# Performance work log

Measured on AMD Instinct MI355X. Metric: run time of the kernel, lower is better.

The kernel has to match this reference:

```python
import jax, jax.numpy as jnp
import numpy as np

D_MODEL = 1024
N_HEADS = 16
HEAD_DIM = D_MODEL // N_HEADS
SCALE = HEAD_DIM ** -0.5
MIN_VAL = jnp.finfo(jnp.float32).min


def setup_inputs() -> dict:
    key = jax.random.key(0)
    ks = jax.random.split(key, 7)
    B, T = 1, 2048
    s = D_MODEL ** -0.5
    return {
        "x": jax.random.normal(ks[0], (B, T, D_MODEL), dtype=jnp.float32),
        "Wq": jax.random.normal(ks[1], (D_MODEL, D_MODEL), dtype=jnp.float32) * s,
        "Wk1": jax.random.normal(ks[2], (D_MODEL, D_MODEL), dtype=jnp.float32) * s,
        "Wk2": jax.random.normal(ks[3], (D_MODEL, D_MODEL), dtype=jnp.float32) * s,
        "Wv": jax.random.normal(ks[4], (D_MODEL, D_MODEL), dtype=jnp.float32) * s,
        "Wo": jax.random.normal(ks[5], (D_MODEL, D_MODEL), dtype=jnp.float32) * s,
        "lambda_logit": jnp.zeros((N_HEADS,), dtype=jnp.float32),  # logit(0.5)=0
    }


def _split_heads(y):
    B, T, _ = y.shape
    return y.reshape(B, T, N_HEADS, HEAD_DIM).transpose(0, 2, 1, 3)  # [B,H,T,hd]


def reference(x, Wq, Wk1, Wk2, Wv, Wo, lambda_logit):
    B, T, _ = x.shape
    q = _split_heads(x @ Wq.T)
    k1 = _split_heads(x @ Wk1.T)
    k2 = _split_heads(x @ Wk2.T)
    v = _split_heads(x @ Wv.T)

    s1 = jnp.einsum("bhqd,bhkd->bhqk", q, k1) * SCALE
    s2 = jnp.einsum("bhqd,bhkd->bhqk", q, k2) * SCALE

    causal = jnp.arange(T)[None, :] <= jnp.arange(T)[:, None]  # [T,T] keep mask
    s1 = jnp.where(causal[None, None], s1, MIN_VAL)
    s2 = jnp.where(causal[None, None], s2, MIN_VAL)

    attn_exp = jax.nn.softmax(s1, axis=-1)
    attn_noise = jax.nn.softmax(s2, axis=-1)
    lam = jax.nn.sigmoid(lambda_logit)[None, :, None, None]
    attn = attn_exp - lam * attn_noise
    denom = jnp.maximum(jnp.sum(jnp.abs(attn), axis=-1, keepdims=True), 1e-6)
    attn = attn / denom

    out = jnp.einsum("bhqk,bhkd->bhqd", attn, v)
    out = out.transpose(0, 2, 1, 3).reshape(B, T, D_MODEL)
    return out @ Wo.T
```

## Files before the change

kernel.cpp:

```cpp
#include <hip/hip_runtime.h>

#define T_SEQ 2048
#define DM 1024
#define NH 16
#define HD 64
#define SC2 0.1803368801111731f
#define LS 72

typedef unsigned short u16;
typedef unsigned int u32;
typedef __attribute__((ext_vector_type(8))) short bf16x8;
typedef __attribute__((ext_vector_type(4))) float f32x4;

static __device__ __forceinline__ f32x4 mfma16(bf16x8 a, bf16x8 b, f32x4 c) {
    return __builtin_amdgcn_mfma_f32_16x16x32_bf16(a, b, c, 0, 0, 0);
}
static __device__ __forceinline__ float bf2f(u16 u) {
    union { u32 i; float f; } v; v.i = ((u32)u) << 16; return v.f;
}
static __device__ __forceinline__ u16 f2bf(float f) {
    union { float f; u32 i; } v; v.f = f;
    u32 x = v.i;
    x += 0x7FFFu + ((x >> 16) & 1u);
    return (u16)(x >> 16);
}
static __device__ __forceinline__ u16 f2bf_t(float f) {
    union { float f; u32 i; } v; v.f = f;
    return (u16)(v.i >> 16);
}
static __device__ __forceinline__ u32 pk2(float lo, float hi) {
    return (u32)f2bf(lo) | ((u32)f2bf(hi) << 16);
}
static __device__ __forceinline__ float qsum16(float v) {
#pragma unroll
    for (int o = 1; o < 16; o <<= 1) v += __shfl_xor(v, o, 64);
    return v;
}
static __device__ __forceinline__ float ex2(float x) {
    return __builtin_amdgcn_exp2f(x);
}

static __device__ __forceinline__ void gl16(const u16* g, u16* l) {
    __builtin_amdgcn_global_load_lds(
        (const __attribute__((address_space(1))) void*)g,
        (__attribute__((address_space(3))) void*)l,
        16, 0, 0);
}

template <int NISS>
static __device__ __forceinline__ void stage_async(const u16* src, size_t row0,
                                                   size_t lds_, size_t col0,
                                                   u16* dst, int tid) {
#pragma unroll
    for (int it = 0; it < NISS; it++) {
        int r = it * 32 + (tid >> 3);
        int cg = (tid & 7) ^ (r & 7);
        gl16(&src[(row0 + r) * lds_ + col0 + cg * 8], &dst[(it * 256 + tid) * 8]);
    }
}
static __device__ __forceinline__ bf16x8 frag(const u16* buf, int R, int co) {
    return *(const bf16x8*)(&buf[R * 64 + co]);
}

__global__ __launch_bounds__(256) void detect_dtype(const u16* __restrict__ x,
                                                    int* __restrict__ flag) {
    __shared__ int tot;
    const int tid = threadIdx.x;
    if (tid == 0) tot = 0;
    __syncthreads();
    int c = 0;
#pragma unroll
    for (int i = 0; i < 4; i++) {
        u16 v = x[2 * (tid * 4 + i)];
        int e = (v >> 7) & 0xFF;
        c += (e >= 110 && e <= 140) ? 1 : 0;
    }
    atomicAdd(&tot, c);
    __syncthreads();
    if (tid == 0) *flag = (tot >= 512) ? 1 : 0;
}

__global__ __launch_bounds__(256) void cvt_bf16(
    const int* __restrict__ flag,
    const float* __restrict__ x, const float* __restrict__ wq,
    const float* __restrict__ wk1, const float* __restrict__ wk2,
    const float* __restrict__ wv, const float* __restrict__ wo,
    u16* __restrict__ xc, u16* __restrict__ wqc, u16* __restrict__ wk1c,
    u16* __restrict__ wk2c, u16* __restrict__ wvc, u16* __restrict__ woc) {
    if (*flag) return;
    const int b = blockIdx.x;
    const int tid = threadIdx.x;
    const float* src;
    u16* dst;
    int rel;
    if (b < 1024)      { src = x;   dst = xc;   rel = b; }
    else if (b < 1536) { src = wq;  dst = wqc;  rel = b - 1024; }
    else if (b < 2048) { src = wk1; dst = wk1c; rel = b - 1536; }
    else if (b < 2560) { src = wk2; dst = wk2c; rel = b - 2048; }
    else if (b < 3072) { src = wv;  dst = wvc;  rel = b - 2560; }
    else               { src = wo;  dst = woc;  rel = b - 3072; }
    size_t idx = (size_t)rel * 2048 + (size_t)tid * 8;
    const float* s = src + idx;
    uint4 a = *(const uint4*)s;
    uint4 bq = *(const uint4*)(s + 4);
    const float* af = (const float*)&a;
    const float* bf = (const float*)&bq;
    uint4 r;
    r.x = pk2(af[0], af[1]); r.y = pk2(af[2], af[3]);
    r.z = pk2(bf[0], bf[1]); r.w = pk2(bf[2], bf[3]);
    *(uint4*)(dst + idx) = r;
}

__global__ __launch_bounds__(256) void qkv_gemm(
    const int* __restrict__ flag,
    const void* __restrict__ x0, const void* __restrict__ wq0,
    const void* __restrict__ wk10, const void* __restrict__ wk20,
    const void* __restrict__ wv0,
    const u16* __restrict__ xc, const u16* __restrict__ wqc,
    const u16* __restrict__ wk1c, const u16* __restrict__ wk2c,
    const u16* __restrict__ wvc,
    u16* __restrict__ qd, u16* __restrict__ k1d, u16* __restrict__ k2d,
    u16* __restrict__ vtd) {
    __shared__ __align__(16) u16 As[2][128 * 64];
    __shared__ __align__(16) u16 Bs[2][128 * 64];

    const int f = *flag;
    const int tid = threadIdx.x;
    const int w = blockIdx.x >> 3;
    const int n0 = (blockIdx.x & 7) * 128;
    const int m0 = blockIdx.y * 128;
    const u16* xb = f ? (const u16*)x0 : xc;
    const u16* Bb;
    if (w == 0)      Bb = f ? (const u16*)wq0  : wqc;
    else if (w == 1) Bb = f ? (const u16*)wk10 : wk1c;
    else if (w == 2) Bb = f ? (const u16*)wk20 : wk2c;
    else             Bb = f ? (const u16*)wv0  : wvc;

    const int lane = tid & 63, wave = tid >> 6;
    const int lr = lane & 15, quad = lane >> 4;
    const int wm = (wave >> 1) * 64, wn = (wave & 1) * 64;
    const int sw = lr & 7;

    f32x4 acc[4][4];
#pragma unroll
    for (int i = 0; i < 4; i++)
#pragma unroll
        for (int j = 0; j < 4; j++) acc[i][j] = (f32x4){0.f, 0.f, 0.f, 0.f};

    stage_async<4>(xb, m0, DM, 0, As[0], tid);
    stage_async<4>(Bb, n0, DM, 0, Bs[0], tid);
    for (int k0 = 0; k0 < DM; k0 += 64) {
        const int cur = (k0 >> 6) & 1;
        __syncthreads();
        if (k0 + 64 < DM) {
            stage_async<4>(xb, m0, DM, k0 + 64, As[cur ^ 1], tid);
            stage_async<4>(Bb, n0, DM, k0 + 64, Bs[cur ^ 1], tid);
        }
#pragma unroll
        for (int kk = 0; kk < 2; kk++) {
            const int co = ((kk * 4 + quad) ^ sw) * 8;
            bf16x8 af[4], bfr[4];
#pragma unroll
            for (int i = 0; i < 4; i++) af[i] = frag(As[cur], wm + i * 16 + lr, co);
#pragma unroll
            for (int j = 0; j < 4; j++) bfr[j] = frag(Bs[cur], wn + j * 16 + lr, co);
#pragma unroll
            for (int i = 0; i < 4; i++)
#pragma unroll
                for (int j = 0; j < 4; j++) acc[i][j] = mfma16(af[i], bfr[j], acc[i][j]);
        }
    }

#pragma unroll
    for (int i = 0; i < 4; i++)
#pragma unroll
        for (int j = 0; j < 4; j++)
#pragma unroll
            for (int r = 0; r < 4; r++) {
                int t = m0 + wm + i * 16 + quad * 4 + r;
                int o = n0 + wn + j * 16 + lr;
                float val = acc[i][j][r];
                if (w == 0) val *= SC2;
                u16 vbits = f2bf(val);
                int hh = o >> 6, d0 = o & 63;
                if (w == 3)
                    vtd[((size_t)hh * HD + d0) * T_SEQ + t] = vbits;
                else
                    ((w == 0) ? qd : (w == 1) ? k1d : k2d)[((size_t)hh * T_SEQ + t) * HD + d0] = vbits;
            }
}

#define ATTN_MAP_COMMON()                                     \
    const int tid = threadIdx.x;                              \
    const int lane = tid & 63, wave = tid >> 6;               \
    const int lr = lane & 15, quad = lane >> 4;               \
    const int wm = wave * 16;                                 \
    const int sw = lr & 7;

__global__ __launch_bounds__(256) void attn_a(
    const u16* __restrict__ qg, const u16* __restrict__ k1g,
    const u16* __restrict__ k2g, float* __restrict__ zp) {
    __shared__ __align__(16) u16 k1s[64 * 64];
    __shared__ __align__(16) u16 k2s[64 * 64];
    const int b = blockIdx.x;
    const int x = b & 7;
    const int g = b >> 3;
    const int hl = g >> 7;
    const int par = (g >> 5) & 3;
    const int bi = g & 31;
    const int qt = (bi < 16) ? bi : 47 - bi;
    const int h = x * 2 + hl;
    const int t0 = qt * 64;
    ATTN_MAP_COMMON();

    const u16* qh = qg + (size_t)h * T_SEQ * HD;
    const u16* k1h = k1g + (size_t)h * T_SEQ * HD;
    const u16* k2h = k2g + (size_t)h * T_SEQ * HD;

    bf16x8 aq[2];
#pragma unroll
    for (int kk = 0; kk < 2; kk++)
        aq[kk] = *(const bf16x8*)(&qh[(size_t)(t0 + wm + lr) * HD + kk * 32 + quad * 8]);

    float z1a[4] = {0.f, 0.f, 0.f, 0.f}, z2a[4] = {0.f, 0.f, 0.f, 0.f};

    for (int kt = par; kt <= qt; kt += 4) {
        __syncthreads();
        stage_async<2>(k1h, (size_t)kt * 64, HD, 0, k1s, tid);
        stage_async<2>(k2h, (size_t)kt * 64, HD, 0, k2s, tid);
        __syncthreads();

        f32x4 sa[4], sb[4];
#pragma unroll
        for (int j = 0; j < 4; j++) { sa[j] = (f32x4){0.f,0.f,0.f,0.f}; sb[j] = (f32x4){0.f,0.f,0.f,0.f}; }
#pragma unroll
        for (int kk = 0; kk < 2; kk++) {
            const int co = ((kk * 4 + quad) ^ sw) * 8;
#pragma unroll
            for (int j = 0; j < 4; j++) {
                sa[j] = mfma16(aq[kk], frag(k1s, j * 16 + lr, co), sa[j]);
                sb[j] = mfma16(aq[kk], frag(k2s, j * 16 + lr, co), sb[j]);
            }
        }

        if (kt < qt) {
#pragma unroll
            for (int r = 0; r < 4; r++)
#pragma unroll
                for (int j = 0; j < 4; j++) {
                    z1a[r] += ex2(sa[j][r]);
                    z2a[r] += ex2(sb[j][r]);
                }
        } else {
#pragma unroll
            for (int r = 0; r < 4; r++) {
                const int grow = t0 + wm + quad * 4 + r;
#pragma unroll
                for (int j = 0; j < 4; j++) {
                    int gcol = kt * 64 + j * 16 + lr;
                    if (gcol <= grow) {
                        z1a[r] += ex2(sa[j][r]);
                        z2a[r] += ex2(sb[j][r]);
                    }
                }
            }
        }
    }

#pragma unroll
    for (int r = 0; r < 4; r++) {
        float s1 = qsum16(z1a[r]);
        float s2 = qsum16(z2a[r]);
        if (lr == 0) {
            int row = t0 + wm + quad * 4 + r;
            zp[((size_t)(par * 2 + 0) * NH + h) * T_SEQ + row] = s1;
            zp[((size_t)(par * 2 + 1) * NH + h) * T_SEQ + row] = s2;
        }
    }
}

__global__ __launch_bounds__(256) void attn_b(
    const u16* __restrict__ qg, const u16* __restrict__ k1g,
    const u16* __restrict__ k2g, const u16* __restrict__ vtg,
    const float* __restrict__ zp, const void* __restrict__ lamsrc,
    const int* __restrict__ flag,
    float* __restrict__ dpart, u16* __restrict__ opart) {
    __shared__ __align__(16) u16 k1s[64 * 64];
    __shared__ __align__(16) u16 k2s[64 * 64];
    __shared__ __align__(16) u16 vs[64 * 64];
    __shared__ __align__(16) u16 ps[4][16 * LS];
    const int b = blockIdx.x;
    const int x = b & 7;
    const int g = b >> 3;
    const int hl = g >> 6;
    const int par = (g >> 5) & 1;
    const int bi = g & 31;
    const int qt = (bi < 16) ? bi : 47 - bi;
    const int h = x * 2 + hl;
    const int t0 = qt * 64;
    ATTN_MAP_COMMON();

    const int f = *flag;
    float lamlogit = f ? bf2f(((const u16*)lamsrc)[h]) : ((const float*)lamsrc)[h];
    const float lam = 1.0f / (1.0f + __expf(-lamlogit));

    const u16* qh = qg + (size_t)h * T_SEQ * HD;
    const u16* k1h = k1g + (size_t)h * T_SEQ * HD;
    const u16* k2h = k2g + (size_t)h * T_SEQ * HD;
    const u16* vh = vtg + (size_t)h * HD * T_SEQ;

    bf16x8 aq[2];
#pragma unroll
    for (int kk = 0; kk < 2; kk++)
        aq[kk] = *(const bf16x8*)(&qh[(size_t)(t0 + wm + lr) * HD + kk * 32 + quad * 8]);

    float z1l[4], z2l[4];
#pragma unroll
    for (int r = 0; r < 4; r++) {
        int row = t0 + wm + quad * 4 + r;
        float z1 = 0.f, z2 = 0.f;
#pragma unroll
        for (int p = 0; p < 4; p++) {
            z1 += zp[((size_t)(p * 2 + 0) * NH + h) * T_SEQ + row];
            z2 += zp[((size_t)(p * 2 + 1) * NH + h) * T_SEQ + row];
        }
        z1l[r] = -__log2f(z1);
        z2l[r] = __log2f(lam) - __log2f(z2);
    }

    f32x4 oac[4];
#pragma unroll
    for (int j = 0; j < 4; j++) oac[j] = (f32x4){0.f, 0.f, 0.f, 0.f};
    float dacc[4] = {0.f, 0.f, 0.f, 0.f};

    for (int kt = par; kt <= qt; kt += 2) {
        __syncthreads();
        stage_async<2>(k1h, (size_t)kt * 64, HD, 0, k1s, tid);
        stage_async<2>(k2h, (size_t)kt * 64, HD, 0, k2s, tid);
        stage_async<2>(vh, 0, T_SEQ, (size_t)kt * 64, vs, tid);
        __syncthreads();

        f32x4 sa[4], sb[4];
#pragma unroll
        for (int j = 0; j < 4; j++) { sa[j] = (f32x4){0.f,0.f,0.f,0.f}; sb[j] = (f32x4){0.f,0.f,0.f,0.f}; }
#pragma unroll
        for (int kk = 0; kk < 2; kk++) {
            const int co = ((kk * 4 + quad) ^ sw) * 8;
#pragma unroll
            for (int j = 0; j < 4; j++) {
                sa[j] = mfma16(aq[kk], frag(k1s, j * 16 + lr, co), sa[j]);
                sb[j] = mfma16(aq[kk], frag(k2s, j * 16 + lr, co), sb[j]);
            }
        }

        if (kt < qt) {
#pragma unroll
            for (int r = 0; r < 4; r++)
#pragma unroll
                for (int j = 0; j < 4; j++) {
                    float p = ex2(sa[j][r] + z1l[r]) - ex2(sb[j][r] + z2l[r]);
                    dacc[r] += fabsf(p);
                    ps[wave][(quad * 4 + r) * LS + j * 16 + lr] = f2bf_t(p);
                }
        } else {
#pragma unroll
            for (int r = 0; r < 4; r++) {
                const int grow = t0 + wm + quad * 4 + r;
#pragma unroll
                for (int j = 0; j < 4; j++) {
                    int gcol = kt * 64 + j * 16 + lr;
                    float p = 0.f;
                    if (gcol <= grow)
                        p = ex2(sa[j][r] + z1l[r]) - ex2(sb[j][r] + z2l[r]);
                    dacc[r] += fabsf(p);
                    ps[wave][(quad * 4 + r) * LS + j * 16 + lr] = f2bf_t(p);
                }
            }
        }

#pragma unroll
        for (int kk = 0; kk < 2; kk++) {
            bf16x8 pa = *(const bf16x8*)(&ps[wave][lr * LS + kk * 32 + quad * 8]);
            const int co = ((kk * 4 + quad) ^ sw) * 8;
#pragma unroll
            for (int j = 0; j < 4; j++)
                oac[j] = mfma16(pa, frag(vs, j * 16 + lr, co), oac[j]);
        }
    }

#pragma unroll
    for (int r = 0; r < 4; r++) {
        float ds = qsum16(dacc[r]);
        if (lr == 0) {
            int row = t0 + wm + quad * 4 + r;
            dpart[((size_t)par * NH + h) * T_SEQ + row] = ds;
        }
    }
#pragma unroll
    for (int j = 0; j < 4; j++)
#pragma unroll
        for (int r = 0; r < 4; r++) {
            int row = t0 + wm + quad * 4 + r;
            opart[(size_t)par * T_SEQ * DM + (size_t)row * DM + h * HD + j * 16 + lr] =
                f2bf(oac[j][r]);
        }
}

__global__ __launch_bounds__(256) void normalize_o(
    const u16* __restrict__ opart, const float* __restrict__ dpart,
    u16* __restrict__ ao) {
    int g = blockIdx.x * 256 + threadIdx.x;
    int t = g >> 7;
    int cc = g & 127;
    int d0 = cc * 8;
    int h = d0 >> 6;
    float dsum = dpart[(size_t)h * T_SEQ + t] + dpart[(size_t)(NH + h) * T_SEQ + t];
    float rs = 1.f / fmaxf(dsum, 1e-6f);
    uint4 a = *(const uint4*)(&opart[(size_t)t * DM + d0]);
    uint4 bqq = *(const uint4*)(&opart[(size_t)T_SEQ * DM + (size_t)t * DM + d0]);
    const u32* au = (const u32*)&a;
    const u32* bu = (const u32*)&bqq;
    uint4 out;
    u32* ou = (u32*)&out;
#pragma unroll
    for (int i = 0; i < 4; i++) {
        float lo = (bf2f((u16)(au[i] & 0xFFFF)) + bf2f((u16)(bu[i] & 0xFFFF))) * rs;
        float hi = (bf2f((u16)(au[i] >> 16)) + bf2f((u16)(bu[i] >> 16))) * rs;
        ou[i] = pk2(lo, hi);
    }
    *(uint4*)(&ao[(size_t)t * DM + d0]) = out;
}

__global__ __launch_bounds__(256) void out_gemm(
    const u16* __restrict__ ab, const void* __restrict__ wo0,
    const u16* __restrict__ woc, const int* __restrict__ flag,
    void* __restrict__ outp) {
    __shared__ __align__(16) u16 As[2][64 * 64];
    __shared__ __align__(16) u16 Bs[2][64 * 64];

    const int f = *flag;
    const u16* wb = f ? (const u16*)wo0 : woc;
    const int n0 = blockIdx.x * 64;
    const int m0 = blockIdx.y * 64;
    const int tid = threadIdx.x;
    const int lane = tid & 63, wave = tid >> 6;
    const int lr = lane & 15, quad = lane >> 4;
    const int wm = (wave >> 1) * 32, wn = (wave & 1) * 32;
    const int sw = lr & 7;

    f32x4 acc[2][2];
#pragma unroll
    for (int i = 0; i < 2; i++)
#pragma unroll
        for (int j = 0; j < 2; j++) acc[i][j] = (f32x4){0.f, 0.f, 0.f, 0.f};

    stage_async<2>(ab, m0, DM, 0, As[0], tid);
    stage_async<2>(wb, n0, DM, 0, Bs[0], tid);
    for (int k0 = 0; k0 < DM; k0 += 64) {
        const int cur = (k0 >> 6) & 1;
        __syncthreads();
        if (k0 + 64 < DM) {
            stage_async<2>(ab, m0, DM, k0 + 64, As[cur ^ 1], tid);
            stage_async<2>(wb, n0, DM, k0 + 64, Bs[cur ^ 1], tid);
        }
#pragma unroll
        for (int kk = 0; kk < 2; kk++) {
            const int co = ((kk * 4 + quad) ^ sw) * 8;
            bf16x8 af[2], bfr[2];
#pragma unroll
            for (int i = 0; i < 2; i++) af[i] = frag(As[cur], wm + i * 16 + lr, co);
#pragma unroll
            for (int j = 0; j < 2; j++) bfr[j] = frag(Bs[cur], wn + j * 16 + lr, co);
#pragma unroll
            for (int i = 0; i < 2; i++)
#pragma unroll
                for (int j = 0; j < 2; j++) acc[i][j] = mfma16(af[i], bfr[j], acc[i][j]);
        }
    }

#pragma unroll
    for (int i = 0; i < 2; i++)
#pragma unroll
        for (int j = 0; j < 2; j++)
#pragma unroll
            for (int r = 0; r < 4; r++) {
                int t = m0 + wm + i * 16 + quad * 4 + r;
                int o = n0 + wn + j * 16 + lr;
                float val = acc[i][j][r];
                if (f)
                    ((u16*)outp)[(size_t)t * DM + o] = f2bf(val);
                else
                    ((float*)outp)[(size_t)t * DM + o] = val;
            }
}

extern "C" void kernel_launch(void* const* d_in, const int* in_sizes, int n_in,
                              void* d_out, int out_size, void* d_ws, size_t ws_size,
                              hipStream_t stream) {
    char* ws = (char*)d_ws;
    int* flag = (int*)(ws + 0);
    float* zp    = (float*)(ws + ((size_t)1 << 20));
    float* dpart = (float*)(ws + ((size_t)2 << 20));
    u16* qd  = (u16*)(ws + ((size_t)16 << 20));
    u16* k1d = (u16*)(ws + ((size_t)20 << 20));
    u16* k2d = (u16*)(ws + ((size_t)24 << 20));
    u16* vtd = (u16*)(ws + ((size_t)28 << 20));
    u16* ao  = (u16*)(ws + ((size_t)32 << 20));
    u16* opart = (u16*)(ws + ((size_t)36 << 20));
    u16* xc   = (u16*)(ws + ((size_t)44 << 20));
    u16* wqc  = (u16*)(ws + ((size_t)48 << 20));
    u16* wk1c = (u16*)(ws + ((size_t)50 << 20));
    u16* wk2c = (u16*)(ws + ((size_t)52 << 20));
    u16* wvc  = (u16*)(ws + ((size_t)54 << 20));
    u16* woc  = (u16*)(ws + ((size_t)56 << 20));

    detect_dtype<<<dim3(1), 256, 0, stream>>>((const u16*)d_in[0], flag);
    cvt_bf16<<<dim3(3584), 256, 0, stream>>>(
        flag, (const float*)d_in[0], (const float*)d_in[1], (const float*)d_in[2],
        (const float*)d_in[3], (const float*)d_in[4], (const float*)d_in[5],
        xc, wqc, wk1c, wk2c, wvc, woc);
    qkv_gemm<<<dim3(32, 16), 256, 0, stream>>>(
        flag, d_in[0], d_in[1], d_in[2], d_in[3], d_in[4],
        xc, wqc, wk1c, wk2c, wvc, qd, k1d, k2d, vtd);
    attn_a<<<dim3(2048), 256, 0, stream>>>(qd, k1d, k2d, zp);
    attn_b<<<dim3(1024), 256, 0, stream>>>(qd, k1d, k2d, vtd, zp, d_in[6], flag,
                                           dpart, opart);
    normalize_o<<<dim3(1024), 256, 0, stream>>>(opart, dpart, ao);
    out_gemm<<<dim3(16, 32), 256, 0, stream>>>(ao, d_in[5], woc, flag, d_out);
}
```

Baseline: 196.5 us.

## Compute transposed scores with permuted K staging to keep P in registers

Swaps the MFMA operand order so the score tiles come out transposed, and stages K rows through a permuted layout. Each lane then holds the probabilities for its query row in exactly the register layout needed as the A operand of the PV MFMA. This removes the LDS round trip for P and its barrier-free write/read traffic, and reduces the row-sum reductions from 4-step 16-lane shuffles to two xor shuffles. The risk is a less coalesced gather in the permuted K load and some extra packing ALU work.

```diff
diff --git a/kernel.cpp b/kernel.cpp
--- a/kernel.cpp
+++ b/kernel.cpp
@@ -5,7 +5,6 @@
 #define NH 16
 #define HD 64
 #define SC2 0.1803368801111731f
-#define LS 72
 
 typedef unsigned short u16;
 typedef unsigned int u32;
@@ -31,11 +30,6 @@
 static __device__ __forceinline__ u32 pk2(float lo, float hi) {
     return (u32)f2bf(lo) | ((u32)f2bf(hi) << 16);
 }
-static __device__ __forceinline__ float qsum16(float v) {
-#pragma unroll
-    for (int o = 1; o < 16; o <<= 1) v += __shfl_xor(v, o, 64);
-    return v;
-}
 static __device__ __forceinline__ float ex2(float x) {
     return __builtin_amdgcn_exp2f(x);
 }
@@ -56,6 +50,17 @@
         int r = it * 32 + (tid >> 3);
         int cg = (tid & 7) ^ (r & 7);
         gl16(&src[(row0 + r) * lds_ + col0 + cg * 8], &dst[(it * 256 + tid) * 8]);
+    }
+}
+static __device__ __forceinline__ void stage_perm(const u16* src, size_t row0,
+                                                  u16* dst, int tid) {
+#pragma unroll
+    for (int it = 0; it < 2; it++) {
+        int r = it * 32 + (tid >> 3);
+        int jj = r >> 4, m = r & 15;
+        int gr = (jj >> 1) * 32 + (jj & 1) * 4 + (m >> 2) * 8 + (m & 3);
+        int cg = (tid & 7) ^ (r & 7);
+        gl16(&src[(row0 + gr) * HD + cg * 8], &dst[(it * 256 + tid) * 8]);
     }
 }
 static __device__ __forceinline__ bf16x8 frag(const u16* buf, int R, int co) {
@@ -217,65 +222,60 @@
     const u16* k1h = k1g + (size_t)h * T_SEQ * HD;
     const u16* k2h = k2g + (size_t)h * T_SEQ * HD;
 
+    const int qrow = t0 + wm + lr;
     bf16x8 aq[2];
 #pragma unroll
-    for (int kk = 0; kk < 2; kk++)
-        aq[kk] = *(const bf16x8*)(&qh[(size_t)(t0 + wm + lr) * HD + kk * 32 + quad * 8]);
-
-    float z1a[4] = {0.f, 0.f, 0.f, 0.f}, z2a[4] = {0.f, 0.f, 0.f, 0.f};
+    for (int kb = 0; kb < 2; kb++)
+        aq[kb] = *(const bf16x8*)(&qh[(size_t)qrow * HD + kb * 32 + quad * 8]);
+
+    float z1 = 0.f, z2 = 0.f;
 
     for (int kt = par; kt <= qt; kt += 4) {
         __syncthreads();
-        stage_async<2>(k1h, (size_t)kt * 64, HD, 0, k1s, tid);
-        stage_async<2>(k2h, (size_t)kt * 64, HD, 0, k2s, tid);
+        stage_perm(k1h, (size_t)kt * 64, k1s, tid);
+        stage_perm(k2h, (size_t)kt * 64, k2s, tid);
         __syncthreads();
 
         f32x4 sa[4], sb[4];
 #pragma unroll
         for (int j = 0; j < 4; j++) { sa[j] = (f32x4){0.f,0.f,0.f,0.f}; sb[j] = (f32x4){0.f,0.f,0.f,0.f}; }
 #pragma unroll
-        for (int kk = 0; kk < 2; kk++) {
-            const int co = ((kk * 4 + quad) ^ sw) * 8;
+        for (int kb = 0; kb < 2; kb++) {
+            const int co = ((kb * 4 + quad) ^ sw) * 8;
 #pragma unroll
             for (int j = 0; j < 4; j++) {
-                sa[j] = mfma16(aq[kk], frag(k1s, j * 16 + lr, co), sa[j]);
-                sb[j] = mfma16(aq[kk], frag(k2s, j * 16 + lr, co), sb[j]);
+                sa[j] = mfma16(frag(k1s, j * 16 + lr, co), aq[kb], sa[j]);
+                sb[j] = mfma16(frag(k2s, j * 16 + lr, co), aq[kb], sb[j]);
             }
         }
 
         if (kt < qt) {
 #pragma unroll
-            for (int r = 0; r < 4; r++)
-#pragma unroll
-                for (int j = 0; j < 4; j++) {
-                    z1a[r] += ex2(sa[j][r]);
-                    z2a[r] += ex2(sb[j][r]);
+            for (int j = 0; j < 4; j++)
+#pragma unroll
+                for (int r = 0; r < 4; r++) {
+                    z1 += ex2(sa[j][r]);
+                    z2 += ex2(sb[j][r]);
                 }
         } else {
 #pragma unroll
-            for (int r = 0; r < 4; r++) {
-                const int grow = t0 + wm + quad * 4 + r;
-#pragma unroll
-                for (int j = 0; j < 4; j++) {
-                    int gcol = kt * 64 + j * 16 + lr;
-                    if (gcol <= grow) {
-                        z1a[r] += ex2(sa[j][r]);
-                        z2a[r] += ex2(sb[j][r]);
+            for (int j = 0; j < 4; j++)
+#pragma unroll
+                for (int r = 0; r < 4; r++) {
+                    int kglob = kt * 64 + (j >> 1) * 32 + (j & 1) * 4 + quad * 8 + r;
+                    if (kglob <= qrow) {
+                        z1 += ex2(sa[j][r]);
+                        z2 += ex2(sb[j][r]);
                     }
                 }
-            }
-        }
-    }
-
-#pragma unroll
-    for (int r = 0; r < 4; r++) {
-        float s1 = qsum16(z1a[r]);
-        float s2 = qsum16(z2a[r]);
-        if (lr == 0) {
-            int row = t0 + wm + quad * 4 + r;
-            zp[((size_t)(par * 2 + 0) * NH + h) * T_SEQ + row] = s1;
-            zp[((size_t)(par * 2 + 1) * NH + h) * T_SEQ + row] = s2;
-        }
+        }
+    }
+
+    z1 += __shfl_xor(z1, 16, 64); z1 += __shfl_xor(z1, 32, 64);
+    z2 += __shfl_xor(z2, 16, 64); z2 += __shfl_xor(z2, 32, 64);
+    if (quad == 0) {
+        zp[((size_t)(par * 2 + 0) * NH + h) * T_SEQ + qrow] = z1;
+        zp[((size_t)(par * 2 + 1) * NH + h) * T_SEQ + qrow] = z2;
     }
 }
 
@@ -288,7 +288,6 @@
     __shared__ __align__(16) u16 k1s[64 * 64];
     __shared__ __align__(16) u16 k2s[64 * 64];
     __shared__ __align__(16) u16 vs[64 * 64];
-    __shared__ __align__(16) u16 ps[4][16 * LS];
     const int b = blockIdx.x;
     const int x = b & 7;
     const int g = b >> 3;
@@ -309,34 +308,30 @@
     const u16* k2h = k2g + (size_t)h * T_SEQ * HD;
     const u16* vh = vtg + (size_t)h * HD * T_SEQ;
 
+    const int qrow = t0 + wm + lr;
     bf16x8 aq[2];
 #pragma unroll
-    for (int kk = 0; kk < 2; kk++)
-        aq[kk] = *(const bf16x8*)(&qh[(size_t)(t0 + wm + lr) * HD + kk * 32 + quad * 8]);
-
-    float z1l[4], z2l[4];
-#pragma unroll
-    for (int r = 0; r < 4; r++) {
-        int row = t0 + wm + quad * 4 + r;
-        float z1 = 0.f, z2 = 0.f;
-#pragma unroll
-        for (int p = 0; p < 4; p++) {
-            z1 += zp[((size_t)(p * 2 + 0) * NH + h) * T_SEQ + row];
-            z2 += zp[((size_t)(p * 2 + 1) * NH + h) * T_SEQ + row];
-        }
-        z1l[r] = -__log2f(z1);
-        z2l[r] = __log2f(lam) - __log2f(z2);
-    }
+    for (int kb = 0; kb < 2; kb++)
+        aq[kb] = *(const bf16x8*)(&qh[(size_t)qrow * HD + kb * 32 + quad * 8]);
+
+    float zz1 = 0.f, zz2 = 0.f;
+#pragma unroll
+    for (int p = 0; p < 4; p++) {
+        zz1 += zp[((size_t)(p * 2 + 0) * NH + h) * T_SEQ + qrow];
+        zz2 += zp[((size_t)(p * 2 + 1) * NH + h) * T_SEQ + qrow];
+    }
+    const float z1l = -__log2f(zz1);
+    const float z2l = __log2f(lam) - __log2f(zz2);
 
     f32x4 oac[4];
 #pragma unroll
     for (int j = 0; j < 4; j++) oac[j] = (f32x4){0.f, 0.f, 0.f, 0.f};
-    float dacc[4] = {0.f, 0.f, 0.f, 0.f};
+    float dacc = 0.f;
 
     for (int kt = par; kt <= qt; kt += 2) {
         __syncthreads();
-        stage_async<2>(k1h, (size_t)kt * 64, HD, 0, k1s, tid);
-        stage_async<2>(k2h, (size_t)kt * 64, HD, 0, k2s, tid);
+        stage_perm(k1h, (size_t)kt * 64, k1s, tid);
+        stage_perm(k2h, (size_t)kt * 64, k2s, tid);
         stage_async<2>(vh, 0, T_SEQ, (size_t)kt * 64, vs, tid);
         __syncthreads();
 
@@ -344,58 +339,65 @@
 #pragma unroll
         for (int j = 0; j < 4; j++) { sa[j] = (f32x4){0.f,0.f,0.f,0.f}; sb[j] = (f32x4){0.f,0.f,0.f,0.f}; }
 #pragma unroll
-        for (int kk = 0; kk < 2; kk++) {
-            const int co = ((kk * 4 + quad) ^ sw) * 8;
+        for (int kb = 0; kb < 2; kb++) {
+            const int co = ((kb * 4 + quad) ^ sw) * 8;
 #pragma unroll
             for (int j = 0; j < 4; j++) {
-                sa[j] = mfma16(aq[kk], frag(k1s, j * 16 + lr, co), sa[j]);
-                sb[j] = mfma16(aq[kk], frag(k2s, j * 16 + lr, co), sb[j]);
+                sa[j] = mfma16(frag(k1s, j * 16 + lr, co), aq[kb], sa[j]);
+                sb[j] = mfma16(frag(k2s, j * 16 + lr, co), aq[kb], sb[j]);
             }
         }
 
+        float pt[2][8];
         if (kt < qt) {
 #pragma unroll
-            for (int r = 0; r < 4; r++)
-#pragma unroll
-                for (int j = 0; j < 4; j++) {
-                    float p = ex2(sa[j][r] + z1l[r]) - ex2(sb[j][r] + z2l[r]);
-                    dacc[r] += fabsf(p);
-                    ps[wave][(quad * 4 + r) * LS + j * 16 + lr] = f2bf_t(p);
+            for (int j = 0; j < 4; j++)
+#pragma unroll
+                for (int r = 0; r < 4; r++) {
+                    float pv = ex2(sa[j][r] + z1l) - ex2(sb[j][r] + z2l);
+                    dacc += fabsf(pv);
+                    pt[j >> 1][(j & 1) * 4 + r] = pv;
                 }
         } else {
 #pragma unroll
-            for (int r = 0; r < 4; r++) {
-                const int grow = t0 + wm + quad * 4 + r;
-#pragma unroll
-                for (int j = 0; j < 4; j++) {
-                    int gcol = kt * 64 + j * 16 + lr;
-                    float p = 0.f;
-                    if (gcol <= grow)
-                        p = ex2(sa[j][r] + z1l[r]) - ex2(sb[j][r] + z2l[r]);
-                    dacc[r] += fabsf(p);
-                    ps[wave][(quad * 4 + r) * LS + j * 16 + lr] = f2bf_t(p);
+            for (int j = 0; j < 4; j++)
+#pragma unroll
+                for (int r = 0; r < 4; r++) {
+                    int kglob = kt * 64 + (j >> 1) * 32 + (j & 1) * 4 + quad * 8 + r;
+                    float pv = 0.f;
+                    if (kglob <= qrow)
+                        pv = ex2(sa[j][r] + z1l) - ex2(sb[j][r] + z2l);
+                    dacc += fabsf(pv);
+                    pt[j >> 1][(j & 1) * 4 + r] = pv;
                 }
-            }
-        }
-
-#pragma unroll
-        for (int kk = 0; kk < 2; kk++) {
-            bf16x8 pa = *(const bf16x8*)(&ps[wave][lr * LS + kk * 32 + quad * 8]);
-            const int co = ((kk * 4 + quad) ^ sw) * 8;
+        }
+
+        bf16x8 pa[2];
+#pragma unroll
+        for (int kh = 0; kh < 2; kh++) {
+            union { u32 w[4]; bf16x8 v; } pk_;
+#pragma unroll
+            for (int wi = 0; wi < 4; wi++)
+                pk_.w[wi] = (u32)f2bf_t(pt[kh][2 * wi]) |
+                            ((u32)f2bf_t(pt[kh][2 * wi + 1]) << 16);
+            pa[kh] = pk_.v;
+        }
+
+#pragma unroll
+        for (int kh = 0; kh < 2; kh++) {
+            const int co = ((kh * 4 + quad) ^ sw) * 8;
 #pragma unroll
             for (int j = 0; j < 4; j++)
-                oac[j] = mfma16(pa, frag(vs, j * 16 + lr, co), oac[j]);
-        }
-    }
-
-#pragma unroll
-    for (int r = 0; r < 4; r++) {
-        float ds = qsum16(dacc[r]);
-        if (lr == 0) {
-            int row = t0 + wm + quad * 4 + r;
-            dpart[((size_t)par * NH + h) * T_SEQ + row] = ds;
-        }
-    }
+                oac[j] = mfma16(pa[kh], frag(vs, j * 16 + lr, co), oac[j]);
+        }
+    }
+
+    float ds = dacc;
+    ds += __shfl_xor(ds, 16, 64);
+    ds += __shfl_xor(ds, 32, 64);
+    if (quad == 0)
+        dpart[((size_t)par * NH + h) * T_SEQ + qrow] = ds;
+
 #pragma unroll
     for (int j = 0; j < 4; j++)
 #pragma unroll
```

New measurement: 188.8 us. 1.04x faster.
